# Performance work log

Measured on AMD Instinct MI355X. Metric: run time of the kernel, lower is better.

## Reference

```python
import jax, jax.numpy as jnp
import numpy as np

B, N, L, D, H = 2, 2048, 2048, 1024, 16
HD = D // H  # 64


def setup_inputs() -> dict:
    key = jax.random.key(0)
    ks = jax.random.split(key, 12)
    s = 0.02
    return {
        "x_q": jax.random.normal(ks[0], (B, N, D), jnp.float32),
        "x_kv": jax.random.normal(ks[1], (B, L, D), jnp.float32),
        "pad_mask": jax.random.randint(ks[2], (B, L), 0, 2) > 0,
        "wq": jax.random.normal(ks[3], (D, D), jnp.float32) * s,
        "bq": jnp.zeros((D,), jnp.float32),
        "wk": jax.random.normal(ks[4], (D, D), jnp.float32) * s,
        "bk": jnp.zeros((D,), jnp.float32),
        "wv": jax.random.normal(ks[5], (D, D), jnp.float32) * s,
        "bv": jnp.zeros((D,), jnp.float32),
        "wo": jax.random.normal(ks[6], (D, D), jnp.float32) * s,
        "bo": jnp.zeros((D,), jnp.float32),
    }


def reference(x_q, x_kv, pad_mask, wq, bq, wk, bk, wv, bv, wo, bo):
    scale = HD ** -0.5
    # projections: (B, S, D) -> (B, H, S, HD)
    def split_heads(x):
        return x.reshape(x.shape[0], x.shape[1], H, HD).transpose(0, 2, 1, 3)
    q = split_heads(x_q @ wq + bq) * scale
    k = split_heads(x_kv @ wk + bk)
    v = split_heads(x_kv @ wv + bv)
    attn = jnp.einsum('bhic,bhjc->bhij', q, k)  # (B, H, N, L)
    neg = -jnp.finfo(attn.dtype).max
    attn = jnp.where(pad_mask[:, None, None, :], neg, attn)
    attn = jax.nn.softmax(attn, axis=-1)
    o = jnp.einsum('bhij,bhjc->bhic', attn, v)  # (B, H, N, HD)
    o = o.transpose(0, 2, 1, 3).reshape(B, N, D)
    return o @ wo + bo
```

## Files before the change

kernel.cpp:

```cpp
#include <hip/hip_runtime.h>
#include <hip/hip_bf16.h>
#include <math.h>

typedef __bf16 bf16;
typedef __attribute__((ext_vector_type(8))) __bf16 bf16x8;
typedef __attribute__((ext_vector_type(4))) __bf16 bf16x4;
typedef __attribute__((ext_vector_type(4))) float floatx4;
typedef __attribute__((ext_vector_type(16))) float floatx16;

#define BB 2
#define NN 2048
#define LL 2048
#define DD 1024
#define HH 16
#define HDD 64

#define QSCALE (0.125f * 1.44269504f)
#define PCLAMP 21.66f
#define MBIAS  (-100000.0f)

__device__ __forceinline__ void async16(const bf16* g, bf16* l) {
  __builtin_amdgcn_global_load_lds((const __attribute__((address_space(1))) void*)(g),
                                   (__attribute__((address_space(3))) void*)(l), 16, 0, 0);
}

__device__ __forceinline__ unsigned cvtpk(float a, float b) {
  unsigned r;
  asm("v_cvt_pk_bf16_f32 %0, %1, %2" : "=v"(r) : "v"(a), "v"(b));
  return r;
}

__device__ __forceinline__ void plswap(unsigned &x, unsigned &y) {
  auto r = __builtin_amdgcn_permlane32_swap(x, y, false, false);
  x = (unsigned)r[0];
  y = (unsigned)r[1];
}

__device__ __forceinline__ bf16x8 mk_frag(unsigned w0, unsigned w1, unsigned w2, unsigned w3) {
  union { unsigned u[4]; bf16x8 b; } f;
  f.u[0] = w0; f.u[1] = w1; f.u[2] = w2; f.u[3] = w3;
  return f.b;
}

__global__ __launch_bounds__(256) void prep_kernel(
    const float* __restrict__ xq, const float* __restrict__ xkv,
    bf16* __restrict__ Xqb, bf16* __restrict__ Xkvb, int nconv, int elemsEach,
    const float* __restrict__ W0, const float* __restrict__ W1,
    const float* __restrict__ W2, const float* __restrict__ W3,
    bf16* __restrict__ T0, bf16* __restrict__ T1,
    bf16* __restrict__ T2, bf16* __restrict__ T3,
    const unsigned* __restrict__ mask, float* __restrict__ biasF)
{
  __shared__ bf16 Tb[64][72];
  const int bid = blockIdx.x;
  const int t = threadIdx.x;

  if (bid < nconv) {
    const int half = nconv >> 1;
    const float* s = (bid < half) ? xq : xkv;
    bf16* d = (bid < half) ? Xqb : Xkvb;
    int gid = (bid < half) ? bid : bid - half;
    int idx = (gid * 256 + t) * 8;
    if (idx >= elemsEach) return;
    floatx4 a = *(const floatx4*)&s[idx];
    floatx4 b = *(const floatx4*)&s[idx + 4];
    bf16x8 o;
#pragma unroll
    for (int e = 0; e < 4; e++) { o[e] = (bf16)a[e]; o[4 + e] = (bf16)b[e]; }
    *(bf16x8*)&d[idx] = o;
    return;
  }
  if (bid < nconv + 1024) {
    const int wb = bid - nconv;
    const int which = wb >> 8;
    const float* W = which == 0 ? W0 : which == 1 ? W1 : which == 2 ? W2 : W3;
    bf16*       T = which == 0 ? T0 : which == 1 ? T1 : which == 2 ? T2 : T3;
    const int tile = wb & 255;
    const int k0 = (tile >> 4) * 64, n0 = (tile & 15) * 64;
    const int r = t >> 2;
    const int c = (t & 3) * 16;
    const float* Wr = W + (size_t)(k0 + r) * 1024 + n0 + c;
    floatx4 f0 = *(const floatx4*)(Wr + 0);
    floatx4 f1 = *(const floatx4*)(Wr + 4);
    floatx4 f2 = *(const floatx4*)(Wr + 8);
    floatx4 f3 = *(const floatx4*)(Wr + 12);
#pragma unroll
    for (int e = 0; e < 4; e++) {
      Tb[c + e][r]      = (bf16)f0[e];
      Tb[c + 4 + e][r]  = (bf16)f1[e];
      Tb[c + 8 + e][r]  = (bf16)f2[e];
      Tb[c + 12 + e][r] = (bf16)f3[e];
    }
    __syncthreads();
    bf16* Tr = T + (size_t)(n0 + r) * 1024 + k0 + c;
    *(bf16x8*)&Tr[0] = *(const bf16x8*)&Tb[r][c];
    *(bf16x8*)&Tr[8] = *(const bf16x8*)&Tb[r][c + 8];
    return;
  }
  __shared__ int hasBig, hasFloat;
  if (t == 0) { hasBig = 0; hasFloat = 0; }
  __syncthreads();
  int big = 0, flt = 0;
  for (int idx = t; idx < 1024; idx += 256) {
    unsigned v = mask[idx];
    if (v == 0x3F800000u) flt = 1;
    else if (v > 1u) big = 1;
  }
  if (big) atomicOr(&hasBig, 1);
  if (flt) atomicOr(&hasFloat, 1);
  __syncthreads();
  const int mode = hasFloat ? 2 : (hasBig ? 1 : 0);
  for (int k = t * 16; k < t * 16 + 16; k++) {
    bool m;
    if (mode == 0)      m = ((const int*)mask)[k] != 0;
    else if (mode == 1) m = ((const unsigned char*)mask)[k] != 0;
    else                m = ((const float*)mask)[k] != 0.0f;
    biasF[k] = m ? MBIAS : 0.0f;
  }
}

template <typename TC>
__device__ __forceinline__ void gemm_body32(
    int bx, const bf16* __restrict__ A, const bf16* __restrict__ Wt,
    const float* __restrict__ bias, TC* __restrict__ C, float scale, int transv)
{
  __shared__ bf16 As[128 * 64];
  __shared__ bf16 Bs[128 * 64];

  const int tm = bx >> 3, tn = bx & 7;
  const int m0 = tm * 128, n0 = tn * 128;
  const int t = threadIdx.x;
  const int w = t >> 6, l = t & 63;
  const int col = l & 31, half = l >> 5;
  const int wm = (w >> 1) * 64, wn = (w & 1) * 64;
  const int sr  = t >> 3;
  const int scl = (t & 7) * 8;
  const int scs = (((t & 7) ^ (sr & 7)) * 8);
  const int csw = col & 7;

  floatx16 acc[2][2];
#pragma unroll
  for (int mi = 0; mi < 2; mi++)
#pragma unroll
    for (int ni = 0; ni < 2; ni++)
#pragma unroll
      for (int e = 0; e < 16; e++) acc[mi][ni][e] = 0.0f;

  for (int k0 = 0; k0 < 1024; k0 += 64) {
    __syncthreads();
#pragma unroll
    for (int j = 0; j < 4; j++)
      async16(&A[(size_t)(m0 + j * 32 + sr) * 1024 + k0 + scs], &As[(j * 32 + sr) * 64 + scl]);
#pragma unroll
    for (int j = 0; j < 4; j++)
      async16(&Wt[(size_t)(n0 + j * 32 + sr) * 1024 + k0 + scs], &Bs[(j * 32 + sr) * 64 + scl]);
    __syncthreads();
#pragma unroll
    for (int kk = 0; kk < 4; kk++) {
      const int ch = ((kk * 2 + half) ^ csw) * 8;
      bf16x8 af[2], bfr[2];
#pragma unroll
      for (int mi = 0; mi < 2; mi++)
        af[mi] = *(const bf16x8*)&As[(wm + mi * 32 + col) * 64 + ch];
#pragma unroll
      for (int ni = 0; ni < 2; ni++)
        bfr[ni] = *(const bf16x8*)&Bs[(wn + ni * 32 + col) * 64 + ch];
#pragma unroll
      for (int mi = 0; mi < 2; mi++)
#pragma unroll
        for (int ni = 0; ni < 2; ni++)
          acc[mi][ni] = __builtin_amdgcn_mfma_f32_32x32x16_bf16(af[mi], bfr[ni], acc[mi][ni], 0, 0, 0);
    }
  }
#pragma unroll
  for (int ni = 0; ni < 2; ni++) {
    int colg = n0 + wn + ni * 32 + col;
    float bv = bias[colg];
#pragma unroll
    for (int mi = 0; mi < 2; mi++) {
      int rbase = m0 + wm + mi * 32 + half * 4;
      if (transv) {
#pragma unroll
        for (int g = 0; g < 4; g++) {
          int key0 = rbase + g * 8;
          int bb = key0 >> 11, key = key0 & 2047;
          bf16x4 v4;
#pragma unroll
          for (int r = 0; r < 4; r++) v4[r] = (bf16)(acc[mi][ni][g * 4 + r] + bv);
          *(bf16x4*)&((bf16*)C)[(size_t)bb * (DD * (size_t)LL) + (size_t)colg * LL + key] = v4;
        }
      } else {
#pragma unroll
        for (int g = 0; g < 4; g++)
#pragma unroll
          for (int r = 0; r < 4; r++)
            C[(size_t)(rbase + g * 8 + r) * 1024 + colg] = (TC)((acc[mi][ni][g * 4 + r] + bv) * scale);
      }
    }
  }
}

__global__ __launch_bounds__(256) void qkv_gemm32(
    const bf16* __restrict__ Xq, const bf16* __restrict__ Xkv,
    const bf16* __restrict__ Wtq, const bf16* __restrict__ Wtk, const bf16* __restrict__ Wtv,
    const float* __restrict__ bq, const float* __restrict__ bk, const float* __restrict__ bv,
    bf16* __restrict__ Qp, bf16* __restrict__ Kp, bf16* __restrict__ VtG, int shift)
{
  const int bid = blockIdx.x;
  const int which = bid >> shift;
  const int bx = bid & ((1 << shift) - 1);
  if (which == 0)      gemm_body32<bf16>(bx, Xq,  Wtq, bq, Qp,  QSCALE, 0);
  else if (which == 1) gemm_body32<bf16>(bx, Xkv, Wtk, bk, Kp,  1.0f,   0);
  else                 gemm_body32<bf16>(bx, Xkv, Wtv, bv, VtG, 1.0f,   1);
}

__global__ __launch_bounds__(256) void out_gemm(
    const bf16* __restrict__ A, const bf16* __restrict__ Wt,
    const float* __restrict__ bias, float* __restrict__ C)
{
  __shared__ bf16 As[128 * 64];
  __shared__ bf16 Bs[64 * 64];

  const int bx = blockIdx.x;
  const int tm = bx >> 4, tn = bx & 15;
  const int m0 = tm * 128, n0 = tn * 64;
  const int t = threadIdx.x;
  const int w = t >> 6, l = t & 63;
  const int q = l >> 4, i = l & 15;
  const int wm = (w >> 1) * 64, wn = (w & 1) * 32;
  const int sr  = t >> 3;
  const int scl = (t & 7) * 8;
  const int scs = (((t & 7) ^ (sr & 7)) * 8);
  const int isw = i & 7;

  const floatx4 zero = {0.f, 0.f, 0.f, 0.f};
  floatx4 acc[4][2];
#pragma unroll
  for (int mi = 0; mi < 4; mi++)
#pragma unroll
    for (int ni = 0; ni < 2; ni++) acc[mi][ni] = zero;

  for (int k0 = 0; k0 < 1024; k0 += 64) {
    __syncthreads();
#pragma unroll
    for (int j = 0; j < 4; j++)
      async16(&A[(size_t)(m0 + j * 32 + sr) * 1024 + k0 + scs], &As[(j * 32 + sr) * 64 + scl]);
#pragma unroll
    for (int j = 0; j < 2; j++)
      async16(&Wt[(size_t)(n0 + j * 32 + sr) * 1024 + k0 + scs], &Bs[(j * 32 + sr) * 64 + scl]);
    __syncthreads();
#pragma unroll
    for (int ks = 0; ks < 2; ks++) {
      const int ch = ((ks * 4 + q) ^ isw) * 8;
      bf16x8 af[4], bfr[2];
#pragma unroll
      for (int mi = 0; mi < 4; mi++)
        af[mi] = *(const bf16x8*)&As[(wm + mi * 16 + i) * 64 + ch];
#pragma unroll
      for (int ni = 0; ni < 2; ni++)
        bfr[ni] = *(const bf16x8*)&Bs[(wn + ni * 16 + i) * 64 + ch];
#pragma unroll
      for (int mi = 0; mi < 4; mi++)
#pragma unroll
        for (int ni = 0; ni < 2; ni++)
          acc[mi][ni] = __builtin_amdgcn_mfma_f32_16x16x32_bf16(af[mi], bfr[ni], acc[mi][ni], 0, 0, 0);
    }
  }
#pragma unroll
  for (int ni = 0; ni < 2; ni++) {
    int colg = n0 + wn + ni * 16 + i;
    float bv = bias[colg];
#pragma unroll
    for (int mi = 0; mi < 4; mi++) {
      int row = m0 + wm + mi * 16 + q * 4;
#pragma unroll
      for (int r = 0; r < 4; r++)
        C[(size_t)(row + r) * 1024 + colg] = acc[mi][ni][r] + bv;
    }
  }
}

__global__ __launch_bounds__(256) void attn_kernel(
    const bf16* __restrict__ Q, const bf16* __restrict__ K,
    const bf16* __restrict__ Vt, const float* __restrict__ biasF,
    bf16* __restrict__ O, int hbits)
{
  __shared__ bf16 Kbuf[4][64 * 64];
  __shared__ bf16 Vbuf[4][64 * 64];

  const int bid = blockIdx.x;
  const int qt = bid >> hbits;
  const int hb = bid & ((1 << hbits) - 1);
  const int h  = (hbits == 5) ? (hb >> 1) : hb;
  const int b  = (hbits == 5) ? (hb & 1) : 0;
  const int t = threadIdx.x;
  const int w = t >> 6, lane = t & 63;
  const int col = lane & 31;
  const int hi  = lane >> 5;
  const int lsw = lane & 7;

  const bf16* Qb = Q  + (size_t)b * (NN * DD) + h * HDD;
  const bf16* Kb = K  + (size_t)b * (LL * DD) + h * HDD;
  const bf16* Vb = Vt + (size_t)b * (DD * (size_t)LL) + (size_t)(h * HDD) * LL;
  const float* biasFb = biasF + b * LL;

  const int qrow = qt * 128 + w * 32;

  bf16x8 qfrag[4];
#pragma unroll
  for (int dc = 0; dc < 4; dc++)
    qfrag[dc] = *(const bf16x8*)&Qb[(size_t)(qrow + col) * DD + dc * 16 + hi * 8];

  floatx16 oacc[2];
#pragma unroll
  for (int db = 0; db < 2; db++)
#pragma unroll
    for (int e = 0; e < 16; e++) oacc[db][e] = 0.0f;
  float psum = 0.0f;

  const int sr  = t >> 3;
  const int scl = (t & 7) * 8;
  const int scs = ((t & 7) ^ (sr & 7)) * 8;

  auto STAGE = [&](int tile, int slot) {
    const int k0 = tile * 64;
    async16(&Kb[(size_t)(k0 + sr) * DD + scs],        &Kbuf[slot][sr * 64 + scl]);
    async16(&Kb[(size_t)(k0 + sr + 32) * DD + scs],   &Kbuf[slot][(sr + 32) * 64 + scl]);
    async16(&Vb[(size_t)sr * LL + k0 + scs],          &Vbuf[slot][sr * 64 + scl]);
    async16(&Vb[(size_t)(sr + 32) * LL + k0 + scs],   &Vbuf[slot][(sr + 32) * 64 + scl]);
  };

  floatx4 pb[2][4];
  bf16x8 pfp[4];
  floatx16 sacc[2];

  auto QK = [&](int slot) {
#pragma unroll
    for (int kb = 0; kb < 2; kb++)
#pragma unroll
      for (int g = 0; g < 4; g++)
#pragma unroll
        for (int rr = 0; rr < 4; rr++)
          sacc[kb][g * 4 + rr] = pb[kb][g][rr];
    __builtin_amdgcn_s_setprio(1);
#pragma unroll
    for (int kb = 0; kb < 2; kb++)
#pragma unroll
      for (int dc = 0; dc < 4; dc++) {
        bf16x8 kf = *(const bf16x8*)&Kbuf[slot][(kb * 32 + col) * 64 + ((dc * 2 + hi) ^ lsw) * 8];
        sacc[kb] = __builtin_amdgcn_mfma_f32_32x32x16_bf16(kf, qfrag[dc], sacc[kb], 0, 0, 0);
      }
  };

  auto PV = [&](int slot) {
#pragma unroll
    for (int db = 0; db < 2; db++)
#pragma unroll
      for (int kc = 0; kc < 4; kc++) {
        bf16x8 vf = *(const bf16x8*)&Vbuf[slot][(db * 32 + col) * 64 + ((kc * 2 + hi) ^ lsw) * 8];
        oacc[db] = __builtin_amdgcn_mfma_f32_32x32x16_bf16(vf, pfp[kc], oacc[db], 0, 0, 0);
      }
    __builtin_amdgcn_s_setprio(0);
  };

  auto SOFTMAX = [&](int nextTile) {
#pragma unroll
    for (int kb = 0; kb < 2; kb++)
#pragma unroll
      for (int hh = 0; hh < 2; hh++) {
        float pv[8];
#pragma unroll
        for (int e = 0; e < 8; e++) {
          float p = __builtin_amdgcn_exp2f(fminf(sacc[kb][hh * 8 + e], PCLAMP));
          psum += p;
          pv[e] = p;
        }
        unsigned a0 = cvtpk(pv[0], pv[1]);
        unsigned a1 = cvtpk(pv[2], pv[3]);
        unsigned b0 = cvtpk(pv[4], pv[5]);
        unsigned b1 = cvtpk(pv[6], pv[7]);
        plswap(a0, b0);
        plswap(a1, b1);
        pfp[kb * 2 + hh] = mk_frag(a0, a1, b0, b1);
      }
    const int kn = (nextTile & 31) * 64;
#pragma unroll
    for (int kb = 0; kb < 2; kb++)
#pragma unroll
      for (int g = 0; g < 4; g++)
        pb[kb][g] = *(const floatx4*)&biasFb[kn + kb * 32 + g * 8 + hi * 4];
  };

#pragma unroll
  for (int kb = 0; kb < 2; kb++)
#pragma unroll
    for (int g = 0; g < 4; g++)
      pb[kb][g] = *(const floatx4*)&biasFb[kb * 32 + g * 8 + hi * 4];
  STAGE(0, 0);
  STAGE(1, 1);

  asm volatile("s_waitcnt vmcnt(4)" ::: "memory");
  __builtin_amdgcn_s_barrier();
  __builtin_amdgcn_sched_barrier(0);

  QK(0);
  __builtin_amdgcn_s_setprio(0);
  SOFTMAX(1);

  const int NT = LL / 64;
  for (int kt = 1; kt < NT; kt++) {
    if (kt + 1 < NT) {
      STAGE(kt + 1, (kt + 1) & 3);
      asm volatile("s_waitcnt vmcnt(4)" ::: "memory");
    } else {
      asm volatile("s_waitcnt vmcnt(0)" ::: "memory");
    }
    __builtin_amdgcn_s_barrier();
    __builtin_amdgcn_sched_barrier(0);
    QK(kt & 3);
    PV((kt - 1) & 3);
    SOFTMAX(kt + 1);
  }
  __builtin_amdgcn_s_setprio(1);
  PV((NT - 1) & 3);

  psum += __shfl_xor(psum, 32, 64);
  float inv = 1.0f / fmaxf(psum, 1e-30f);

  bf16* Ob = O + (size_t)b * (NN * DD) + h * HDD;
#pragma unroll
  for (int db = 0; db < 2; db++)
#pragma unroll
    for (int g = 0; g < 4; g++) {
      bf16x4 v4;
#pragma unroll
      for (int rr = 0; rr < 4; rr++) v4[rr] = (bf16)(oacc[db][g * 4 + rr] * inv);
      *(bf16x4*)&Ob[(size_t)(qrow + col) * DD + db * 32 + g * 8 + hi * 4] = v4;
    }
}

extern "C" void kernel_launch(void* const* d_in, const int* in_sizes, int n_in,
                              void* d_out, int out_size, void* d_ws, size_t ws_size,
                              hipStream_t stream)
{
  const float* x_q  = (const float*)d_in[0];
  const float* x_kv = (const float*)d_in[1];
  const void*  pad  = d_in[2];
  const float* wq = (const float*)d_in[3];
  const float* bq = (const float*)d_in[4];
  const float* wk = (const float*)d_in[5];
  const float* bk = (const float*)d_in[6];
  const float* wv = (const float*)d_in[7];
  const float* bv = (const float*)d_in[8];
  const float* wo = (const float*)d_in[9];
  const float* bo = (const float*)d_in[10];
  float* out = (float*)d_out;

  char* ws = (char*)d_ws;
  const size_t MB = (size_t)1 << 20;
  const size_t fullElems = (size_t)BB * NN * DD;
  const size_t batchElems = (size_t)NN * DD;

  if (ws_size >= 49 * MB) {
    bf16* Xqb   = (bf16*)(ws);
    bf16* Xkvb  = (bf16*)(ws + 8 * MB);
    bf16* Wtq   = (bf16*)(ws + 16 * MB);
    bf16* Wtk   = (bf16*)(ws + 18 * MB);
    bf16* Wtv   = (bf16*)(ws + 20 * MB);
    bf16* Wto   = (bf16*)(ws + 22 * MB);
    bf16* Qp    = (bf16*)(ws + 24 * MB);
    bf16* Kp    = (bf16*)(ws + 32 * MB);
    bf16* VtG   = (bf16*)(ws + 40 * MB);
    float* biasF = (float*)(ws + 48 * MB);
    bf16* Op    = Xqb;

    prep_kernel<<<5121, 256, 0, stream>>>(x_q, x_kv, Xqb, Xkvb, 4096, (int)fullElems,
                                          wq, wk, wv, wo, Wtq, Wtk, Wtv, Wto,
                                          (const unsigned*)pad, biasF);
    qkv_gemm32<<<768, 256, 0, stream>>>(Xqb, Xkvb, Wtq, Wtk, Wtv, bq, bk, bv, Qp, Kp, VtG, 8);
    attn_kernel<<<512, 256, 0, stream>>>(Qp, Kp, VtG, biasF, Op, 5);
    out_gemm<<<512, 256, 0, stream>>>(Op, Wto, bo, out);
  } else {
    bf16* Wtq   = (bf16*)(ws);
    bf16* Wtk   = (bf16*)(ws + 2 * MB);
    bf16* Wtv   = (bf16*)(ws + 4 * MB);
    bf16* Wto   = (bf16*)(ws + 6 * MB);
    bf16* Xqb   = (bf16*)(ws + 8 * MB);
    bf16* Xkvb  = (bf16*)(ws + 12 * MB);
    bf16* Qp    = (bf16*)(ws + 16 * MB);
    bf16* Kp    = (bf16*)(ws + 20 * MB);
    bf16* VtG   = (bf16*)(ws + 24 * MB);
    float* biasF = (float*)(ws + 28 * MB);
    bf16* Op    = Xqb;

    for (int b = 0; b < BB; b++) {
      if (b == 0)
        prep_kernel<<<3073, 256, 0, stream>>>(x_q, x_kv, Xqb, Xkvb, 2048, (int)batchElems,
                                              wq, wk, wv, wo, Wtq, Wtk, Wtv, Wto,
                                              (const unsigned*)pad, biasF);
      else
        prep_kernel<<<2048, 256, 0, stream>>>(x_q + b * batchElems, x_kv + b * batchElems,
                                              Xqb, Xkvb, 2048, (int)batchElems,
                                              wq, wk, wv, wo, Wtq, Wtk, Wtv, Wto,
                                              (const unsigned*)pad, biasF);
      qkv_gemm32<<<384, 256, 0, stream>>>(Xqb, Xkvb, Wtq, Wtk, Wtv, bq, bk, bv, Qp, Kp, VtG, 7);
      attn_kernel<<<256, 256, 0, stream>>>(Qp, Kp, VtG, biasF + b * LL, Op, 4);
      out_gemm<<<256, 256, 0, stream>>>(Op, Wto, bo, out + b * batchElems);
    }
  }
}
```

Before: 225.2 us.

## Triple-buffer GEMM tiles with async LDS loads and remap block order

Both projection GEMMs (QKV and output) switch from a single-buffered 64-wide K tile with two barriers per step to a three-stage ring of 32-wide K tiles. The next tile's global-to-LDS async loads are issued before computing on the current one, using vmcnt waits and a single barrier per step, so memory latency overlaps with MFMA work. The swizzle pattern is adjusted to the narrower rows. Block indices are also remapped so that consecutive blocks are strided across the tile grid, likely for better L2/cache locality. The single barrier before overwriting stage (k+1)%3 relies on the three-deep ring for correctness.

```diff
diff --git a/kernel.cpp b/kernel.cpp
--- a/kernel.cpp
+++ b/kernel.cpp
@@ -124,8 +124,8 @@
     int bx, const bf16* __restrict__ A, const bf16* __restrict__ Wt,
     const float* __restrict__ bias, TC* __restrict__ C, float scale, int transv)
 {
-  __shared__ bf16 As[128 * 64];
-  __shared__ bf16 Bs[128 * 64];
+  __shared__ bf16 As[3][128 * 32];
+  __shared__ bf16 Bs[3][128 * 32];
 
   const int tm = bx >> 3, tn = bx & 7;
   const int m0 = tm * 128, n0 = tn * 128;
@@ -133,10 +133,10 @@
   const int w = t >> 6, l = t & 63;
   const int col = l & 31, half = l >> 5;
   const int wm = (w >> 1) * 64, wn = (w & 1) * 64;
-  const int sr  = t >> 3;
-  const int scl = (t & 7) * 8;
-  const int scs = (((t & 7) ^ (sr & 7)) * 8);
-  const int csw = col & 7;
+  const int sr  = t >> 2;
+  const int scl = (t & 3) * 8;
+  const int scs = (((t & 3) ^ ((t >> 3) & 3)) * 8);
+  const int csw = (col >> 1) & 3;
 
   floatx16 acc[2][2];
 #pragma unroll
@@ -146,25 +146,36 @@
 #pragma unroll
       for (int e = 0; e < 16; e++) acc[mi][ni][e] = 0.0f;
 
-  for (int k0 = 0; k0 < 1024; k0 += 64) {
-    __syncthreads();
-#pragma unroll
-    for (int j = 0; j < 4; j++)
-      async16(&A[(size_t)(m0 + j * 32 + sr) * 1024 + k0 + scs], &As[(j * 32 + sr) * 64 + scl]);
-#pragma unroll
-    for (int j = 0; j < 4; j++)
-      async16(&Wt[(size_t)(n0 + j * 32 + sr) * 1024 + k0 + scs], &Bs[(j * 32 + sr) * 64 + scl]);
-    __syncthreads();
-#pragma unroll
-    for (int kk = 0; kk < 4; kk++) {
+  auto STAGE = [&](int k0, int s) {
+    async16(&A[(size_t)(m0 + sr) * 1024 + k0 + scs],       &As[s][sr * 32 + scl]);
+    async16(&A[(size_t)(m0 + 64 + sr) * 1024 + k0 + scs],  &As[s][(64 + sr) * 32 + scl]);
+    async16(&Wt[(size_t)(n0 + sr) * 1024 + k0 + scs],      &Bs[s][sr * 32 + scl]);
+    async16(&Wt[(size_t)(n0 + 64 + sr) * 1024 + k0 + scs], &Bs[s][(64 + sr) * 32 + scl]);
+  };
+
+  STAGE(0, 0);
+  const int NK = 1024 / 32;
+  for (int k = 0; k < NK; k++) {
+    if (k + 1 < NK) {
+      STAGE((k + 1) * 32, (k + 1) % 3);
+      asm volatile("s_waitcnt vmcnt(4)" ::: "memory");
+    } else {
+      asm volatile("s_waitcnt vmcnt(0)" ::: "memory");
+    }
+    __builtin_amdgcn_s_barrier();
+    __builtin_amdgcn_sched_barrier(0);
+    const bf16* as = &As[k % 3][0];
+    const bf16* bs = &Bs[k % 3][0];
+#pragma unroll
+    for (int kk = 0; kk < 2; kk++) {
       const int ch = ((kk * 2 + half) ^ csw) * 8;
       bf16x8 af[2], bfr[2];
 #pragma unroll
       for (int mi = 0; mi < 2; mi++)
-        af[mi] = *(const bf16x8*)&As[(wm + mi * 32 + col) * 64 + ch];
+        af[mi] = *(const bf16x8*)&as[(wm + mi * 32 + col) * 32 + ch];
 #pragma unroll
       for (int ni = 0; ni < 2; ni++)
-        bfr[ni] = *(const bf16x8*)&Bs[(wn + ni * 32 + col) * 64 + ch];
+        bfr[ni] = *(const bf16x8*)&bs[(wn + ni * 32 + col) * 32 + ch];
 #pragma unroll
       for (int mi = 0; mi < 2; mi++)
 #pragma unroll
@@ -208,7 +219,9 @@
 {
   const int bid = blockIdx.x;
   const int which = bid >> shift;
-  const int bx = bid & ((1 << shift) - 1);
+  const int bx0 = bid & ((1 << shift) - 1);
+  const int q = (1 << shift) >> 3;
+  const int bx = (bx0 & 7) * q + (bx0 >> 3);
   if (which == 0)      gemm_body32<bf16>(bx, Xq,  Wtq, bq, Qp,  QSCALE, 0);
   else if (which == 1) gemm_body32<bf16>(bx, Xkv, Wtk, bk, Kp,  1.0f,   0);
   else                 gemm_body32<bf16>(bx, Xkv, Wtv, bv, VtG, 1.0f,   1);
@@ -218,20 +231,22 @@
     const bf16* __restrict__ A, const bf16* __restrict__ Wt,
     const float* __restrict__ bias, float* __restrict__ C)
 {
-  __shared__ bf16 As[128 * 64];
-  __shared__ bf16 Bs[64 * 64];
-
-  const int bx = blockIdx.x;
+  __shared__ bf16 As[3][128 * 32];
+  __shared__ bf16 Bs[3][64 * 32];
+
+  const int bid = blockIdx.x;
+  const int qs = gridDim.x >> 3;
+  const int bx = (bid & 7) * qs + (bid >> 3);
   const int tm = bx >> 4, tn = bx & 15;
   const int m0 = tm * 128, n0 = tn * 64;
   const int t = threadIdx.x;
   const int w = t >> 6, l = t & 63;
   const int q = l >> 4, i = l & 15;
   const int wm = (w >> 1) * 64, wn = (w & 1) * 32;
-  const int sr  = t >> 3;
-  const int scl = (t & 7) * 8;
-  const int scs = (((t & 7) ^ (sr & 7)) * 8);
-  const int isw = i & 7;
+  const int sr  = t >> 2;
+  const int scl = (t & 3) * 8;
+  const int scs = (((t & 3) ^ ((t >> 3) & 3)) * 8);
+  const int isw = (i >> 1) & 3;
 
   const floatx4 zero = {0.f, 0.f, 0.f, 0.f};
   floatx4 acc[4][2];
@@ -240,31 +255,38 @@
 #pragma unroll
     for (int ni = 0; ni < 2; ni++) acc[mi][ni] = zero;
 
-  for (int k0 = 0; k0 < 1024; k0 += 64) {
-    __syncthreads();
-#pragma unroll
-    for (int j = 0; j < 4; j++)
-      async16(&A[(size_t)(m0 + j * 32 + sr) * 1024 + k0 + scs], &As[(j * 32 + sr) * 64 + scl]);
-#pragma unroll
-    for (int j = 0; j < 2; j++)
-      async16(&Wt[(size_t)(n0 + j * 32 + sr) * 1024 + k0 + scs], &Bs[(j * 32 + sr) * 64 + scl]);
-    __syncthreads();
-#pragma unroll
-    for (int ks = 0; ks < 2; ks++) {
-      const int ch = ((ks * 4 + q) ^ isw) * 8;
-      bf16x8 af[4], bfr[2];
-#pragma unroll
-      for (int mi = 0; mi < 4; mi++)
-        af[mi] = *(const bf16x8*)&As[(wm + mi * 16 + i) * 64 + ch];
+  auto STAGE = [&](int k0, int s) {
+    async16(&A[(size_t)(m0 + sr) * 1024 + k0 + scs],       &As[s][sr * 32 + scl]);
+    async16(&A[(size_t)(m0 + 64 + sr) * 1024 + k0 + scs],  &As[s][(64 + sr) * 32 + scl]);
+    async16(&Wt[(size_t)(n0 + sr) * 1024 + k0 + scs],      &Bs[s][sr * 32 + scl]);
+  };
+
+  STAGE(0, 0);
+  const int NK = 1024 / 32;
+  for (int k = 0; k < NK; k++) {
+    if (k + 1 < NK) {
+      STAGE((k + 1) * 32, (k + 1) % 3);
+      asm volatile("s_waitcnt vmcnt(3)" ::: "memory");
+    } else {
+      asm volatile("s_waitcnt vmcnt(0)" ::: "memory");
+    }
+    __builtin_amdgcn_s_barrier();
+    __builtin_amdgcn_sched_barrier(0);
+    const bf16* as = &As[k % 3][0];
+    const bf16* bs = &Bs[k % 3][0];
+    const int ch = (q ^ isw) * 8;
+    bf16x8 af[4], bfr[2];
+#pragma unroll
+    for (int mi = 0; mi < 4; mi++)
+      af[mi] = *(const bf16x8*)&as[(wm + mi * 16 + i) * 32 + ch];
+#pragma unroll
+    for (int ni = 0; ni < 2; ni++)
+      bfr[ni] = *(const bf16x8*)&bs[(wn + ni * 16 + i) * 32 + ch];
+#pragma unroll
+    for (int mi = 0; mi < 4; mi++)
 #pragma unroll
       for (int ni = 0; ni < 2; ni++)
-        bfr[ni] = *(const bf16x8*)&Bs[(wn + ni * 16 + i) * 64 + ch];
-#pragma unroll
-      for (int mi = 0; mi < 4; mi++)
-#pragma unroll
-        for (int ni = 0; ni < 2; ni++)
-          acc[mi][ni] = __builtin_amdgcn_mfma_f32_16x16x32_bf16(af[mi], bfr[ni], acc[mi][ni], 0, 0, 0);
-    }
+        acc[mi][ni] = __builtin_amdgcn_mfma_f32_16x16x32_bf16(af[mi], bfr[ni], acc[mi][ni], 0, 0, 0);
   }
 #pragma unroll
   for (int ni = 0; ni < 2; ni++) {
```

Result: faster. 217.3 us (-3.5%).
